# Performance work log

Measured on AMD Instinct MI355X. Metric: run time of the kernel, lower is better.

## Reference

```python
import jax, jax.numpy as jnp
import numpy as np

D_MODEL = 2048
D_HEAD = 128
N_HEADS = D_MODEL // D_HEAD
SEQ_LENS = (512, 768, 384, 384)  # packed varlen sequences, sum = 2048
L_TOTAL = sum(SEQ_LENS)
EPS = 1e-6


def setup_inputs() -> dict:
    key = jax.random.key(0)
    ks = jax.random.split(key, 8)
    x = jax.random.normal(ks[0], (L_TOTAL, D_MODEL), jnp.float32)
    # Flux-style rope table: pairwise-duplicated cos/sin, pe = concat([cos, sin], -1) -> (L, 2*d_head)
    half = D_HEAD // 2
    pos = np.arange(L_TOTAL, dtype=np.float32)[:, None]
    freqs = 1.0 / (10000.0 ** (np.arange(half, dtype=np.float32) / half))  # (half,)
    ang = pos * freqs[None, :]                      # (L, half)
    cos = np.repeat(np.cos(ang), 2, axis=-1)        # (L, d_head), duplicated per pair
    sin = np.repeat(np.sin(ang), 2, axis=-1)
    pe = jnp.asarray(np.concatenate([cos, sin], axis=-1))  # (L, 2*d_head)
    seq_lens = jnp.asarray(SEQ_LENS, dtype=jnp.int32)
    std = 0.02
    qkv_w = std * jax.random.truncated_normal(ks[1], -2.0, 2.0, (3 * D_MODEL, D_MODEL), jnp.float32)
    qkv_b = jnp.zeros((3 * D_MODEL,), jnp.float32)
    q_scale = jnp.ones((D_HEAD,), jnp.float32)
    k_scale = jnp.ones((D_HEAD,), jnp.float32)
    proj_w = std * jax.random.truncated_normal(ks[2], -2.0, 2.0, (D_MODEL, D_MODEL), jnp.float32)
    proj_b = jnp.zeros((D_MODEL,), jnp.float32)
    return {"x": x, "pe": pe, "seq_lens": seq_lens, "qkv_w": qkv_w, "qkv_b": qkv_b,
            "q_scale": q_scale, "k_scale": k_scale, "proj_w": proj_w, "proj_b": proj_b}


def _rms_norm(t, scale):
    tf = t.astype(jnp.float32)
    rrms = jax.lax.rsqrt(jnp.mean(tf * tf, axis=-1, keepdims=True) + EPS)
    return (tf * rrms * scale).astype(t.dtype)


def _apply_rope(t, pe):
    # t: (L, nh, dh); pe: (L, 2*dh) with pairwise-duplicated cos|sin
    L, nh, dh = t.shape
    c = pe[:, None, 0:dh:2]     # (L, 1, dh/2) per-pair cos
    s = pe[:, None, dh::2]      # (L, 1, dh/2) per-pair sin
    tr = t.reshape(L, nh, dh // 2, 2)
    t1, t2 = tr[..., 0], tr[..., 1]
    out = jnp.stack([t1 * c - t2 * s, t1 * s + t2 * c], axis=-1)
    return out.reshape(L, nh, dh)


def reference(x, pe, seq_lens, qkv_w, qkv_b, q_scale, k_scale, proj_w, proj_b):
    L = x.shape[0]
    qkv = x @ qkv_w.T + qkv_b                      # (L, 3*D)
    q, k, v = jnp.split(qkv, 3, axis=-1)
    q = q.reshape(L, N_HEADS, D_HEAD)
    k = k.reshape(L, N_HEADS, D_HEAD)
    v = v.reshape(L, N_HEADS, D_HEAD)
    q = _rms_norm(q, q_scale)
    k = _rms_norm(k, k_scale)
    q = _apply_rope(q, pe)
    k = _apply_rope(k, pe)
    # block-diagonal (packed varlen) attention
    n = seq_lens.shape[0]
    seg = jnp.repeat(jnp.arange(n, dtype=jnp.int32), seq_lens, total_repeat_length=L)  # (L,)
    mask = seg[:, None] == seg[None, :]            # (L, L) block-diagonal
    scale = 1.0 / jnp.sqrt(jnp.float32(D_HEAD))
    scores = jnp.einsum('lhd,mhd->hlm', q, k) * scale  # (nh, L, L)
    scores = jnp.where(mask[None], scores, jnp.finfo(scores.dtype).min)
    p = jax.nn.softmax(scores, axis=-1)
    out = jnp.einsum('hlm,mhd->lhd', p, v)         # (L, nh, dh)
    out = out.reshape(L, D_MODEL)
    return out @ proj_w.T + proj_b
```

## Files before the change

### kernel.cpp

```cpp
#include <hip/hip_runtime.h>

typedef unsigned short ushort_t;
typedef __attribute__((ext_vector_type(4))) float f4;
typedef __attribute__((ext_vector_type(8))) short s8v;
typedef __attribute__((ext_vector_type(8))) __bf16 bf8v;

#define AS1 __attribute__((address_space(1)))
#define AS3 __attribute__((address_space(3)))

__device__ __forceinline__ void async16(void* lds, const void* g) {
    __builtin_amdgcn_global_load_lds((AS1 const void*)g, (AS3 void*)lds, 16, 0, 0);
}

__device__ __forceinline__ f4 mfma16(s8v a, s8v b, f4 c) {
    return __builtin_amdgcn_mfma_f32_16x16x32_bf16(
        __builtin_bit_cast(bf8v, a), __builtin_bit_cast(bf8v, b), c, 0, 0, 0);
}

__device__ __forceinline__ ushort_t f2bf(float f) {
    unsigned int u = __float_as_uint(f);
    u += 0x7fffu + ((u >> 16) & 1u);
    return (ushort_t)(u >> 16);
}
__device__ __forceinline__ float bf2f(ushort_t u) {
    return __uint_as_float(((unsigned int)u) << 16);
}

#define L_TOT   2048
#define DMODEL  2048
#define DHEAD   128
#define NHEADS  16

__global__ __launch_bounds__(256) void cast_all(const float* __restrict__ x,
                                                const float* __restrict__ w1,
                                                ushort_t* __restrict__ xo,
                                                ushort_t* __restrict__ w1o) {
    for (int i = blockIdx.x * 256 + threadIdx.x; i < 4194304; i += 2048 * 256) {
        const float* src; ushort_t* dst; int off;
        if (i < 1048576)      { src = x;  dst = xo;  off = 0; }
        else                  { src = w1; dst = w1o; off = 1048576; }
        int j = i - off;
        float4 v = ((const float4*)src)[j];
        ushort4 o;
        o.x = f2bf(v.x); o.y = f2bf(v.y); o.z = f2bf(v.z); o.w = f2bf(v.w);
        ((ushort4*)dst)[j] = o;
    }
}


template <int P>
__device__ __forceinline__ void cluster(f4 (&acc)[8][4], const s8v (&af)[2][2],
                                        const s8v (&bf)[4][2]) {
    __builtin_amdgcn_s_setprio(1);
#pragma unroll
    for (int mm = 0; mm < 2; mm++)
#pragma unroll
        for (int nn = 0; nn < 4; nn++) {
            acc[2 * P + mm][nn] = mfma16(af[mm][0], bf[nn][0], acc[2 * P + mm][nn]);
            acc[2 * P + mm][nn] = mfma16(af[mm][1], bf[nn][1], acc[2 * P + mm][nn]);
        }
    __builtin_amdgcn_s_setprio(0);
}

#define LDF(base, row, oo) (*(const s8v*)&(base)[(row) * 64 + (oo)])

#define STG(dst, gb, Tt, h)                                                              \
    async16(&(dst)[tid * 8 + (2 * (h)) * 4096],                                          \
            (gb) + (size_t)(Tt) * 64 + (size_t)(128 * (h)) * K);                         \
    async16(&(dst)[tid * 8 + (2 * (h) + 1) * 4096],                                      \
            (gb) + (size_t)(Tt) * 64 + (size_t)(128 * (h) + 64) * K);

#define OPENB()                                                                          \
    __builtin_amdgcn_s_barrier();                                                        \
    asm volatile("s_waitcnt lgkmcnt(0)" ::: "memory");                                   \
    __builtin_amdgcn_sched_barrier(0);

#define TILE(cur, T)                                                                     \
    {                                                                                    \
        const int Tn1 = ((T) + 1 < NT) ? (T) + 1 : NT - 1;                               \
        const int Tn2 = ((T) + 2 < NT) ? (T) + 2 : NT - 1;                               \
        const ushort_t* fA = stA[cur];                                                   \
        const ushort_t* fB = stB[cur];                                                   \
        s8v bfrag[4][2];                                                                 \
        s8v afrag[2][2];                                                                 \
                                                                  \
        bfrag[0][0] = LDF(fB, brow + 0,  o0); bfrag[0][1] = LDF(fB, brow + 0,  o1);      \
        bfrag[1][0] = LDF(fB, brow + 16, o0); bfrag[1][1] = LDF(fB, brow + 16, o1);      \
        bfrag[2][0] = LDF(fB, brow + 32, o0); bfrag[2][1] = LDF(fB, brow + 32, o1);      \
        bfrag[3][0] = LDF(fB, brow + 48, o0); bfrag[3][1] = LDF(fB, brow + 48, o1);      \
        afrag[0][0] = LDF(fA, arow + 0,  o0); afrag[0][1] = LDF(fA, arow + 0,  o1);      \
        afrag[1][0] = LDF(fA, arow + 16, o0); afrag[1][1] = LDF(fA, arow + 16, o1);      \
        STG(stA[(cur) ^ 1], gA, Tn1, 0)                                                  \
        OPENB()                                                                          \
        cluster<0>(acc, afrag, bfrag);                                                   \
        __builtin_amdgcn_s_barrier();                                                    \
                                                                  \
        afrag[0][0] = LDF(fA, arow + 32, o0); afrag[0][1] = LDF(fA, arow + 32, o1);      \
        afrag[1][0] = LDF(fA, arow + 48, o0); afrag[1][1] = LDF(fA, arow + 48, o1);      \
        STG(stA[(cur) ^ 1], gA, Tn1, 1)                                                  \
        OPENB()                                                                          \
        cluster<1>(acc, afrag, bfrag);                                                   \
        __builtin_amdgcn_s_barrier();                                                    \
                                                                  \
        afrag[0][0] = LDF(fA, arow + 64, o0); afrag[0][1] = LDF(fA, arow + 64, o1);      \
        afrag[1][0] = LDF(fA, arow + 80, o0); afrag[1][1] = LDF(fA, arow + 80, o1);      \
        STG(stB[cur], gB, Tn2, 0)                                                        \
        OPENB()                                                                          \
        cluster<2>(acc, afrag, bfrag);                                                   \
        __builtin_amdgcn_s_barrier();                                                    \
                                                                  \
        afrag[0][0] = LDF(fA, arow + 96,  o0); afrag[0][1] = LDF(fA, arow + 96,  o1);    \
        afrag[1][0] = LDF(fA, arow + 112, o0); afrag[1][1] = LDF(fA, arow + 112, o1);    \
        STG(stB[cur], gB, Tn2, 1)                                                        \
        asm volatile("s_waitcnt vmcnt(4)" ::: "memory");                                 \
        __builtin_amdgcn_sched_barrier(0);                                               \
        OPENB()                                                                          \
        cluster<3>(acc, afrag, bfrag);                                                   \
        __builtin_amdgcn_s_barrier();                                                    \
    }

__global__ __launch_bounds__(512, 2) void gemm_qkv256(const ushort_t* __restrict__ A,
                                                      const ushort_t* __restrict__ Bt,
                                                      const float* __restrict__ bias,
                                                      const float* __restrict__ projw,
                                                      ushort_t* __restrict__ projw_bf,
                                                      ushort_t* __restrict__ qk_out,
                                                      ushort_t* __restrict__ vt_out,
                                                      int K) {
    __shared__ alignas(16) ushort_t sA[2][16384];
    __shared__ alignas(16) ushort_t sB[2][16384];

    const int tid  = threadIdx.x;
    const int lane = tid & 63;
    const int wave = tid >> 6;
    const int wm = wave >> 2;
    const int wn = wave & 3;

    const int phys = blockIdx.y * 8 + blockIdx.x;
    const int lid  = (phys & 7) * 32 + (phys >> 3);
    const int xcd  = lid >> 5;
    const int slot = lid & 31;

    if (slot >= 24) {
        const int ci = xcd * 8 + (slot - 24);
#pragma unroll
        for (int it = 0; it < 32; it++) {
            int j = ci * 16384 + it * 512 + tid;
            float4 v = ((const float4*)projw)[j];
            ushort4 o;
            o.x = f2bf(v.x); o.y = f2bf(v.y); o.z = f2bf(v.z); o.w = f2bf(v.w);
            ((ushort4*)projw_bf)[j] = o;
        }
        return;
    }

    const int gid = xcd * 24 + slot;
    const int bxs = gid & 7;
    const int bys = gid >> 3;

    const int bm = bxs * 256;
    const int bn = bys * 256;
    const bool is_v = bys >= 16;
    const int NT = K >> 6;

    const int q15 = lane & 15;
    const int g   = lane >> 4;
    const int l7  = lane & 7;
    const int o0  = ((g    ) ^ l7) * 8;
    const int o1  = ((g + 4) ^ l7) * 8;
    const int arow = wm * 128 + q15;
    const int brow = wn * 64 + q15;

    const int rs  = tid >> 3;
    const int csw = ((tid & 7) ^ (rs & 7)) * 8;
    const ushort_t* Abase = A  + (size_t)(bm + rs) * K + csw;
    const ushort_t* Bbase = Bt + (size_t)(bn + rs) * K + csw;

    ushort_t* stA[2]; ushort_t* stB[2];
    const ushort_t* gA; const ushort_t* gB;
    if (!is_v) { stA[0] = sA[0]; stA[1] = sA[1]; stB[0] = sB[0]; stB[1] = sB[1];
                 gA = Abase; gB = Bbase; }
    else       { stA[0] = sB[0]; stA[1] = sB[1]; stB[0] = sA[0]; stB[1] = sA[1];
                 gA = Bbase; gB = Abase; }

    f4 acc[8][4];
#pragma unroll
    for (int i = 0; i < 8; i++)
#pragma unroll
        for (int j = 0; j < 4; j++) acc[i][j] = (f4){0.f, 0.f, 0.f, 0.f};

    STG(stA[0], gA, 0, 0) STG(stA[0], gA, 0, 1)
    STG(stB[0], gB, 0, 0) STG(stB[0], gB, 0, 1)
    {
        const int T1 = NT > 1 ? 1 : 0;
        STG(stB[1], gB, T1, 0) STG(stB[1], gB, T1, 1)
    }
    asm volatile("s_waitcnt vmcnt(4)" ::: "memory");
    __builtin_amdgcn_sched_barrier(0);
    __builtin_amdgcn_s_barrier();

    for (int T = 0; T < NT; T += 2) {
        TILE(0, T)
        TILE(1, T + 1)
    }

    if (!is_v) {
#pragma unroll
        for (int n = 0; n < 4; n++) {
            int col = bn + wn * 64 + n * 16 + q15;
            float bv = bias[col];
#pragma unroll
            for (int m = 0; m < 8; m++) {
                int r0 = bm + wm * 128 + m * 16 + g * 4;
#pragma unroll
                for (int r = 0; r < 4; r++)
                    qk_out[(size_t)(r0 + r) * 4096 + col] = f2bf(acc[m][n][r] + bv);
            }
        }
    } else {
        const int cb   = (bys - 16) * 256 + wm * 128;
        const int tok0 = bm + wn * 64 + q15;
#pragma unroll
        for (int m = 0; m < 8; m++) {
#pragma unroll
            for (int r = 0; r < 4; r++) {
                int c = cb + m * 16 + g * 4 + r;
                float bv = bias[4096 + c];
#pragma unroll
                for (int n = 0; n < 4; n++)
                    vt_out[(size_t)c * L_TOT + tok0 + n * 16] = f2bf(acc[m][n][r] + bv);
            }
        }
    }
}

__global__ __launch_bounds__(256) void gemm_proj(const ushort_t* __restrict__ A,
                                                 const ushort_t* __restrict__ Bt,
                                                 float* __restrict__ Cf,
                                                 int K) {
    __shared__ alignas(16) ushort_t pA[128 * 64];
    __shared__ alignas(16) ushort_t pB[128 * 64];
    const int tid  = threadIdx.x;
    const int lane = tid & 63;
    const int wave = tid >> 6;
    const int wr = (wave >> 1) * 64;
    const int wc = (wave & 1) * 64;
    const int bm = blockIdx.x * 128;
    const int bn = blockIdx.y * 128;

    f4 acc[4][4];
#pragma unroll
    for (int i = 0; i < 4; i++)
#pragma unroll
        for (int j = 0; j < 4; j++) acc[i][j] = (f4){0.f, 0.f, 0.f, 0.f};

    const int rs  = tid >> 3;
    const int csw = ((tid & 7) ^ (rs & 7)) * 8;
    const ushort_t* Abase = A  + (size_t)(bm + rs) * K + csw;
    const ushort_t* Bbase = Bt + (size_t)(bn + rs) * K + csw;
    const int arow = wr + (lane & 15);
    const int brow = wc + (lane & 15);
    const int l7 = lane & 7;
    const int o0 = (((lane >> 4)    ) ^ l7) * 8;
    const int o1 = (((lane >> 4) + 4) ^ l7) * 8;
    const int kbeg = blockIdx.z * (K >> 1);
    const int kend = kbeg + (K >> 1);

    for (int k0 = kbeg; k0 < kend; k0 += 64) {
#pragma unroll
        for (int s = 0; s < 4; s++) {
            async16(&pA[tid * 8 + s * 2048], Abase + k0 + (size_t)(32 * s) * K);
            async16(&pB[tid * 8 + s * 2048], Bbase + k0 + (size_t)(32 * s) * K);
        }
        __syncthreads();

        s8v af[4], bfr[4];
#pragma unroll
        for (int i = 0; i < 4; i++) af[i]  = *(const s8v*)&pA[(arow + i * 16) * 64 + o0];
#pragma unroll
        for (int j = 0; j < 4; j++) bfr[j] = *(const s8v*)&pB[(brow + j * 16) * 64 + o0];
#pragma unroll
        for (int i = 0; i < 4; i++)
#pragma unroll
            for (int j = 0; j < 4; j++) acc[i][j] = mfma16(af[i], bfr[j], acc[i][j]);

#pragma unroll
        for (int i = 0; i < 4; i++) af[i]  = *(const s8v*)&pA[(arow + i * 16) * 64 + o1];
#pragma unroll
        for (int j = 0; j < 4; j++) bfr[j] = *(const s8v*)&pB[(brow + j * 16) * 64 + o1];
#pragma unroll
        for (int i = 0; i < 4; i++)
#pragma unroll
            for (int j = 0; j < 4; j++) acc[i][j] = mfma16(af[i], bfr[j], acc[i][j]);
        __syncthreads();
    }

    const int q = lane & 15;
    const int g = lane >> 4;
    const int crow0 = bm + wr + g * 4;
    const int ccol0 = bn + wc + q;
    float* Cp = Cf + (size_t)blockIdx.z * L_TOT * DMODEL;
#pragma unroll
    for (int j = 0; j < 4; j++) {
        int col = ccol0 + j * 16;
#pragma unroll
        for (int i = 0; i < 4; i++) {
#pragma unroll
            for (int r = 0; r < 4; r++)
                Cp[(size_t)(crow0 + i * 16 + r) * DMODEL + col] = acc[i][j][r];
        }
    }
}

__global__ __launch_bounds__(256) void reduce_bias(const float* __restrict__ part,
                                                   const float* __restrict__ bias,
                                                   float* __restrict__ out) {
    int i = blockIdx.x * 256 + threadIdx.x;
    f4 a = ((const f4*)part)[i];
    f4 b = ((const f4*)(part + (size_t)L_TOT * DMODEL))[i];
    f4 bv = ((const f4*)bias)[i & 511];
    ((f4*)out)[i] = a + b + bv;
}

__global__ __launch_bounds__(256) void norm_rope(const ushort_t* __restrict__ qk,
                                                 const float* __restrict__ pe,
                                                 const float* __restrict__ q_scale,
                                                 const float* __restrict__ k_scale,
                                                 ushort_t* __restrict__ qh,
                                                 ushort_t* __restrict__ kh) {
    int wid  = blockIdx.x * 4 + (threadIdx.x >> 6);
    int lane = threadIdx.x & 63;
    int l = wid >> 4;
    int h = wid & 15;

    const ushort_t* base = qk + (size_t)l * 4096 + h * DHEAD + 2 * lane;
    ushort2 qu = *(const ushort2*)base;
    ushort2 ku = *(const ushort2*)(base + 2048);
    float qvx = bf2f(qu.x), qvy = bf2f(qu.y);
    float kvx = bf2f(ku.x), kvy = bf2f(ku.y);

    float qss = qvx * qvx + qvy * qvy;
    float kss = kvx * kvx + kvy * kvy;
#pragma unroll
    for (int m = 32; m >= 1; m >>= 1) {
        qss += __shfl_xor(qss, m);
        kss += __shfl_xor(kss, m);
    }
    float qr = rsqrtf(qss * (1.0f / DHEAD) + 1e-6f);
    float kr = rsqrtf(kss * (1.0f / DHEAD) + 1e-6f);

    float c = pe[(size_t)l * 256 + 2 * lane];
    float s = pe[(size_t)l * 256 + 128 + 2 * lane];

    float q1 = qvx * qr * q_scale[2 * lane];
    float q2 = qvy * qr * q_scale[2 * lane + 1];
    float k1 = kvx * kr * k_scale[2 * lane];
    float k2 = kvy * kr * k_scale[2 * lane + 1];

    const float sc = 0.08838834764831845f;
    float qo0 = (q1 * c - q2 * s) * sc;
    float qo1 = (q1 * s + q2 * c) * sc;
    float ko0 = k1 * c - k2 * s;
    float ko1 = k1 * s + k2 * c;

    size_t o = ((size_t)h * L_TOT + l) * DHEAD + 2 * lane;
    ushort2 qp, kp;
    qp.x = f2bf(qo0); qp.y = f2bf(qo1);
    kp.x = f2bf(ko0); kp.y = f2bf(ko1);
    *(ushort2*)(qh + o) = qp;
    *(ushort2*)(kh + o) = kp;
}

__global__ __launch_bounds__(256) void attn_kernel(const ushort_t* __restrict__ qh,
                                                   const ushort_t* __restrict__ kh,
                                                   const ushort_t* __restrict__ vt,
                                                   ushort_t* __restrict__ attn_out) {
    __shared__ alignas(16) ushort_t sK[2][64 * 128];
    __shared__ alignas(16) ushort_t sV[2][128 * 64];
    __shared__ alignas(16) ushort_t sP[4][16 * 64];

    const int phys = blockIdx.y * 32 + blockIdx.x;
    const int lid  = (phys & 7) * 64 + (phys >> 3);
    const int qt = lid & 31;
    const int h  = lid >> 5;

    const int tid = threadIdx.x;
    const int lane = tid & 63;
    const int w = tid >> 6;
    const int qrow0 = qt * 64 + w * 16;

    int q0 = qt * 64;
    int seg_start, seg_end;
    if (q0 < 512)       { seg_start = 0;    seg_end = 512;  }
    else if (q0 < 1280) { seg_start = 512;  seg_end = 1280; }
    else if (q0 < 1664) { seg_start = 1280; seg_end = 1664; }
    else                { seg_start = 1664; seg_end = 2048; }

    const int g = lane >> 4;
    const int q = lane & 15;
    const int qa7 = q & 7;

    const ushort_t* ksrc[4];
    const ushort_t* vsrc[4];
#pragma unroll
    for (int i = 0; i < 4; i++) {
        int p = i * 256 + tid;
        ksrc[i] = kh + ((size_t)h * L_TOT + (p >> 4)) * DHEAD + ((p & 15) ^ ((p >> 4) & 7)) * 8;
        vsrc[i] = vt + ((size_t)h * DHEAD + (p >> 3)) * L_TOT + ((p & 7) ^ ((p >> 3) & 7)) * 8;
    }

    s8v qf[4];
    {
        const ushort_t* qbase = qh + ((size_t)h * L_TOT + qrow0 + q) * DHEAD;
#pragma unroll
        for (int kd = 0; kd < 4; kd++) qf[kd] = *(const s8v*)(qbase + kd * 32 + g * 8);
    }

    f4 o[8];
#pragma unroll
    for (int j = 0; j < 8; j++) o[j] = (f4){0.f, 0.f, 0.f, 0.f};
    float lsum[4] = {0.f, 0.f, 0.f, 0.f};

#pragma unroll
    for (int i = 0; i < 4; i++) {
        int p = i * 256 + tid;
        async16(&sK[0][p * 8], ksrc[i] + (size_t)seg_start * DHEAD);
        async16(&sV[0][p * 8], vsrc[i] + seg_start);
    }

    int cur = 0;
    for (int kt = seg_start; kt < seg_end; kt += 64) {
        if (kt + 64 < seg_end) {
#pragma unroll
            for (int i = 0; i < 4; i++) {
                int p = i * 256 + tid;
                async16(&sK[cur ^ 1][p * 8], ksrc[i] + (size_t)(kt + 64) * DHEAD);
                async16(&sV[cur ^ 1][p * 8], vsrc[i] + (kt + 64));
            }
            asm volatile("s_waitcnt vmcnt(8)" ::: "memory");
        } else {
            asm volatile("s_waitcnt vmcnt(0)" ::: "memory");
        }
        __builtin_amdgcn_sched_barrier(0);
        __syncthreads();

        const ushort_t* Kc = sK[cur];
        const ushort_t* Vc = sV[cur];

        f4 S[4];
        __builtin_amdgcn_s_setprio(1);
#pragma unroll
        for (int tj = 0; tj < 4; tj++) {
            f4 st = (f4){0.f, 0.f, 0.f, 0.f};
#pragma unroll
            for (int kd = 0; kd < 4; kd++) {
                s8v bfrag = *(const s8v*)&Kc[(tj * 16 + q) * 128 + (((kd * 4 + g) ^ qa7) * 8)];
                st = mfma16(qf[kd], bfrag, st);
            }
            S[tj] = st;
        }
        __builtin_amdgcn_s_setprio(0);

#pragma unroll
        for (int tj = 0; tj < 4; tj++)
#pragma unroll
            for (int r = 0; r < 4; r++) {
                float p = __expf(S[tj][r]);
                S[tj][r] = p;
                lsum[r] += p;
            }

#pragma unroll
        for (int tj = 0; tj < 4; tj++) {
            int cg = tj * 2 + (q >> 3);
#pragma unroll
            for (int r = 0; r < 4; r++) {
                int prow = g * 4 + r;
                sP[w][prow * 64 + ((cg ^ (prow & 7)) * 8) + qa7] = f2bf(S[tj][r]);
            }
        }
        asm volatile("s_waitcnt lgkmcnt(0)" ::: "memory");

        __builtin_amdgcn_s_setprio(1);
#pragma unroll
        for (int ks = 0; ks < 2; ks++) {
            s8v pf = *(const s8v*)&sP[w][q * 64 + (((ks * 4 + g) ^ qa7) * 8)];
#pragma unroll
            for (int j = 0; j < 8; j++) {
                s8v vf = *(const s8v*)&Vc[(j * 16 + q) * 64 + (((ks * 4 + g) ^ qa7) * 8)];
                o[j] = mfma16(pf, vf, o[j]);
            }
        }
        __builtin_amdgcn_s_setprio(0);
        __syncthreads();
        cur ^= 1;
    }

#pragma unroll
    for (int r = 0; r < 4; r++) {
        float rs = lsum[r];
        rs += __shfl_xor(rs, 1);
        rs += __shfl_xor(rs, 2);
        rs += __shfl_xor(rs, 4);
        rs += __shfl_xor(rs, 8);
        int row = qrow0 + g * 4 + r;
        float inv = 1.0f / rs;
#pragma unroll
        for (int j = 0; j < 8; j++) {
            attn_out[(size_t)row * DMODEL + h * DHEAD + j * 16 + q] = f2bf(o[j][r] * inv);
        }
    }
}

extern "C" void kernel_launch(void* const* d_in, const int* in_sizes, int n_in,
                              void* d_out, int out_size, void* d_ws, size_t ws_size,
                              hipStream_t stream) {
    const float* x       = (const float*)d_in[0];
    const float* pe      = (const float*)d_in[1];
    const float* qkv_w   = (const float*)d_in[3];
    const float* qkv_b   = (const float*)d_in[4];
    const float* q_scale = (const float*)d_in[5];
    const float* k_scale = (const float*)d_in[6];
    const float* proj_w  = (const float*)d_in[7];
    const float* proj_b  = (const float*)d_in[8];
    float* out = (float*)d_out;

    char* ws = (char*)d_ws;
    const size_t MB = 1024 * 1024;
    ushort_t* x_bf     = (ushort_t*)(ws + 0);
    ushort_t* wqkv_bf  = (ushort_t*)(ws + 8 * MB);
    ushort_t* wproj_bf = (ushort_t*)(ws + 32 * MB);
    ushort_t* qk_bf    = (ushort_t*)(ws + 40 * MB);
    ushort_t* qh       = (ushort_t*)(ws + 57 * MB);
    ushort_t* kh       = (ushort_t*)(ws + 65 * MB);
    ushort_t* vt       = (ushort_t*)(ws + 73 * MB);
    ushort_t* attn_b   = (ushort_t*)(ws + 81 * MB);
    float*    part     = (float*)   (ws + 40 * MB);

    cast_all<<<2048, 256, 0, stream>>>(x, qkv_w, x_bf, wqkv_bf);

    gemm_qkv256<<<dim3(8, 32), 512, 0, stream>>>(x_bf, wqkv_bf, qkv_b,
                                                 proj_w, wproj_bf,
                                                 qk_bf, vt, 2048);

    norm_rope<<<8192, 256, 0, stream>>>(qk_bf, pe, q_scale, k_scale, qh, kh);

    attn_kernel<<<dim3(32, 16), 256, 0, stream>>>(qh, kh, vt, attn_b);

    gemm_proj<<<dim3(16, 16, 2), 256, 0, stream>>>(attn_b, wproj_bf, part, 2048);
    reduce_bias<<<4096, 256, 0, stream>>>(part, proj_b, out);
}
```

Measured before the change: 248.9 us.

## Rewrite projection GEMM with 256x256 double-buffered tiles and 4-way split-K

Replaces the 128x128 single-buffered projection GEMM (2-way split-K) with a 512-thread, 256x256 tile kernel. It reuses the STG/TILE double-buffered pipeline macros from the QKV GEMM, adds XCD-aware block remapping, and splits K four ways into two partial buffers. The reduction kernel now sums four partials plus bias. The aim is more data reuse per block and load/compute overlap, at the cost of more partial-sum traffic and fewer, larger blocks (256 total).

Result: slower. 257.0 us (+3.3%).

```diff
diff --git a/kernel.cpp b/kernel.cpp
--- a/kernel.cpp
+++ b/kernel.cpp
@@ -234,92 +234,92 @@
     }
 }
 
-__global__ __launch_bounds__(256) void gemm_proj(const ushort_t* __restrict__ A,
-                                                 const ushort_t* __restrict__ Bt,
-                                                 float* __restrict__ Cf,
-                                                 int K) {
-    __shared__ alignas(16) ushort_t pA[128 * 64];
-    __shared__ alignas(16) ushort_t pB[128 * 64];
+__global__ __launch_bounds__(512, 2) void gemm_proj256(const ushort_t* __restrict__ A,
+                                                       const ushort_t* __restrict__ Bt,
+                                                       float* __restrict__ pAB,
+                                                       float* __restrict__ pCD,
+                                                       int K) {
+    __shared__ alignas(16) ushort_t sA[2][16384];
+    __shared__ alignas(16) ushort_t sB[2][16384];
+
     const int tid  = threadIdx.x;
     const int lane = tid & 63;
     const int wave = tid >> 6;
-    const int wr = (wave >> 1) * 64;
-    const int wc = (wave & 1) * 64;
-    const int bm = blockIdx.x * 128;
-    const int bn = blockIdx.y * 128;
-
-    f4 acc[4][4];
-#pragma unroll
-    for (int i = 0; i < 4; i++)
-#pragma unroll
-        for (int j = 0; j < 4; j++) acc[i][j] = (f4){0.f, 0.f, 0.f, 0.f};
+    const int wm = wave >> 2;
+    const int wn = wave & 3;
+
+    const int phys = (blockIdx.z * 8 + blockIdx.y) * 8 + blockIdx.x;
+    const int lid  = (phys & 7) * 32 + (phys >> 3);
+    const int bxs  = lid & 7;
+    const int bys  = (lid >> 3) & 7;
+    const int z    = lid >> 6;
+
+    const int bm = bxs * 256;
+    const int bn = bys * 256;
+    const int NT = K >> 6;
+    const int T0 = z * 8;
+
+    const int q15 = lane & 15;
+    const int g   = lane >> 4;
+    const int l7  = lane & 7;
+    const int o0  = ((g    ) ^ l7) * 8;
+    const int o1  = ((g + 4) ^ l7) * 8;
+    const int arow = wm * 128 + q15;
+    const int brow = wn * 64 + q15;
 
     const int rs  = tid >> 3;
     const int csw = ((tid & 7) ^ (rs & 7)) * 8;
-    const ushort_t* Abase = A  + (size_t)(bm + rs) * K + csw;
-    const ushort_t* Bbase = Bt + (size_t)(bn + rs) * K + csw;
-    const int arow = wr + (lane & 15);
-    const int brow = wc + (lane & 15);
-    const int l7 = lane & 7;
-    const int o0 = (((lane >> 4)    ) ^ l7) * 8;
-    const int o1 = (((lane >> 4) + 4) ^ l7) * 8;
-    const int kbeg = blockIdx.z * (K >> 1);
-    const int kend = kbeg + (K >> 1);
-
-    for (int k0 = kbeg; k0 < kend; k0 += 64) {
-#pragma unroll
-        for (int s = 0; s < 4; s++) {
-            async16(&pA[tid * 8 + s * 2048], Abase + k0 + (size_t)(32 * s) * K);
-            async16(&pB[tid * 8 + s * 2048], Bbase + k0 + (size_t)(32 * s) * K);
-        }
-        __syncthreads();
-
-        s8v af[4], bfr[4];
-#pragma unroll
-        for (int i = 0; i < 4; i++) af[i]  = *(const s8v*)&pA[(arow + i * 16) * 64 + o0];
-#pragma unroll
-        for (int j = 0; j < 4; j++) bfr[j] = *(const s8v*)&pB[(brow + j * 16) * 64 + o0];
-#pragma unroll
-        for (int i = 0; i < 4; i++)
-#pragma unroll
-            for (int j = 0; j < 4; j++) acc[i][j] = mfma16(af[i], bfr[j], acc[i][j]);
-
-#pragma unroll
-        for (int i = 0; i < 4; i++) af[i]  = *(const s8v*)&pA[(arow + i * 16) * 64 + o1];
-#pragma unroll
-        for (int j = 0; j < 4; j++) bfr[j] = *(const s8v*)&pB[(brow + j * 16) * 64 + o1];
-#pragma unroll
-        for (int i = 0; i < 4; i++)
-#pragma unroll
-            for (int j = 0; j < 4; j++) acc[i][j] = mfma16(af[i], bfr[j], acc[i][j]);
-        __syncthreads();
-    }
-
-    const int q = lane & 15;
-    const int g = lane >> 4;
-    const int crow0 = bm + wr + g * 4;
-    const int ccol0 = bn + wc + q;
-    float* Cp = Cf + (size_t)blockIdx.z * L_TOT * DMODEL;
-#pragma unroll
-    for (int j = 0; j < 4; j++) {
-        int col = ccol0 + j * 16;
-#pragma unroll
-        for (int i = 0; i < 4; i++) {
+    const ushort_t* gA = A  + (size_t)(bm + rs) * K + csw;
+    const ushort_t* gB = Bt + (size_t)(bn + rs) * K + csw;
+
+    ushort_t* stA[2] = { sA[0], sA[1] };
+    ushort_t* stB[2] = { sB[0], sB[1] };
+
+    f4 acc[8][4];
+#pragma unroll
+    for (int i = 0; i < 8; i++)
+#pragma unroll
+        for (int j = 0; j < 4; j++) acc[i][j] = (f4){0.f, 0.f, 0.f, 0.f};
+
+    STG(stA[0], gA, T0, 0) STG(stA[0], gA, T0, 1)
+    STG(stB[0], gB, T0, 0) STG(stB[0], gB, T0, 1)
+    STG(stB[1], gB, T0 + 1, 0) STG(stB[1], gB, T0 + 1, 1)
+    asm volatile("s_waitcnt vmcnt(4)" ::: "memory");
+    __builtin_amdgcn_sched_barrier(0);
+    __builtin_amdgcn_s_barrier();
+
+    for (int T = T0; T < T0 + 8; T += 2) {
+        TILE(0, T)
+        TILE(1, T + 1)
+    }
+
+    float* dst = (z < 2 ? pAB + (size_t)z * (L_TOT * DMODEL)
+                        : pCD + (size_t)(z - 2) * (L_TOT * DMODEL));
+#pragma unroll
+    for (int n = 0; n < 4; n++) {
+        int col = bn + wn * 64 + n * 16 + q15;
+#pragma unroll
+        for (int m = 0; m < 8; m++) {
+            int r0 = bm + wm * 128 + m * 16 + g * 4;
 #pragma unroll
             for (int r = 0; r < 4; r++)
-                Cp[(size_t)(crow0 + i * 16 + r) * DMODEL + col] = acc[i][j][r];
-        }
-    }
-}
-
-__global__ __launch_bounds__(256) void reduce_bias(const float* __restrict__ part,
-                                                   const float* __restrict__ bias,
-                                                   float* __restrict__ out) {
+                dst[(size_t)(r0 + r) * DMODEL + col] = acc[m][n][r];
+        }
+    }
+}
+
+__global__ __launch_bounds__(256) void reduce_bias4(const float* __restrict__ pAB,
+                                                    const float* __restrict__ pCD,
+                                                    const float* __restrict__ bias,
+                                                    float* __restrict__ out) {
     int i = blockIdx.x * 256 + threadIdx.x;
-    f4 a = ((const f4*)part)[i];
-    f4 b = ((const f4*)(part + (size_t)L_TOT * DMODEL))[i];
+    const size_t PL = (size_t)L_TOT * DMODEL / 4;
+    f4 a = ((const f4*)pAB)[i];
+    f4 b = ((const f4*)pAB)[i + PL];
+    f4 c = ((const f4*)pCD)[i];
+    f4 d = ((const f4*)pCD)[i + PL];
     f4 bv = ((const f4*)bias)[i & 511];
-    ((f4*)out)[i] = a + b + bv;
+    ((f4*)out)[i] = (a + b) + (c + d) + bv;
 }
 
 __global__ __launch_bounds__(256) void norm_rope(const ushort_t* __restrict__ qk,
@@ -535,7 +535,8 @@
     ushort_t* kh       = (ushort_t*)(ws + 65 * MB);
     ushort_t* vt       = (ushort_t*)(ws + 73 * MB);
     ushort_t* attn_b   = (ushort_t*)(ws + 81 * MB);
-    float*    part     = (float*)   (ws + 40 * MB);
+    float*    pAB      = (float*)   (ws + 0);
+    float*    pCD      = (float*)   (ws + 40 * MB);
 
     cast_all<<<2048, 256, 0, stream>>>(x, qkv_w, x_bf, wqkv_bf);
 
@@ -547,6 +548,6 @@
 
     attn_kernel<<<dim3(32, 16), 256, 0, stream>>>(qh, kh, vt, attn_b);
 
-    gemm_proj<<<dim3(16, 16, 2), 256, 0, stream>>>(attn_b, wproj_bf, part, 2048);
-    reduce_bias<<<4096, 256, 0, stream>>>(part, proj_b, out);
-}
+    gemm_proj256<<<dim3(8, 8, 4), 512, 0, stream>>>(attn_b, wproj_bf, pAB, pCD, 2048);
+    reduce_bias4<<<4096, 256, 0, stream>>>(pAB, pCD, proj_b, out);
+}
```
